# Optimization experiments

Measured on AMD Instinct MI355X. Metric: run time of the kernel, lower is better.

Reference implementation:

```python
import jax, jax.numpy as jnp
import numpy as np

N_HEAD = 16
NEG_INF = jnp.float32(-1e30)


def setup_inputs() -> dict:
    key = jax.random.key(0)
    k1, k2, k3 = jax.random.split(key, 3)
    B, T, C = 2, 2048, 1024
    x = jax.random.normal(k1, (B, T, C), dtype=jnp.float32)
    attn_mask = jnp.ones((B, T), dtype=jnp.int32)
    W_qkv = jax.random.normal(k2, (C, 3 * C), dtype=jnp.float32) * (1.0 / np.sqrt(C))
    b_qkv = jnp.zeros((3 * C,), dtype=jnp.float32)
    W_proj = jax.random.normal(k3, (C, C), dtype=jnp.float32) * (1.0 / np.sqrt(C))
    b_proj = jnp.zeros((C,), dtype=jnp.float32)
    return {"x": x, "attn_mask": attn_mask, "W_qkv": W_qkv, "b_qkv": b_qkv,
            "W_proj": W_proj, "b_proj": b_proj}


def reference(x, attn_mask, W_qkv, b_qkv, W_proj, b_proj):
    B, T, C = x.shape
    H = N_HEAD
    hd = C // H
    qkv = x @ W_qkv + b_qkv                       # [B,T,3C]
    q, k, v = jnp.split(qkv, 3, axis=-1)
    q = q.reshape(B, T, H, hd).transpose(0, 2, 1, 3)  # [B,H,T,hd]
    k = k.reshape(B, T, H, hd).transpose(0, 2, 1, 3)
    v = v.reshape(B, T, H, hd).transpose(0, 2, 1, 3)
    att = jnp.einsum('bhqd,bhkd->bhqk', q, k) / jnp.float32(np.sqrt(hd))  # [B,H,T,T]
    causal = jnp.tril(jnp.ones((T, T), dtype=bool))[None, None]           # [1,1,T,T]
    pad = (attn_mask != 0)[:, None, None, :]                              # [B,1,1,T]
    att = jnp.where(causal & pad, att, NEG_INF)
    att = jax.nn.softmax(att, axis=-1)
    y = jnp.einsum('bhqk,bhkd->bhqd', att, v)     # [B,H,T,hd]
    y = y.transpose(0, 2, 1, 3).reshape(B, T, C)
    return y @ W_proj + b_proj
```

## Files before the change

### kernel.cpp

```cpp
#include <hip/hip_runtime.h>

#define T_SEQ 2048
#define NHEAD 16
#define HD 64
#define CDIM 1024

typedef __bf16 bf16x8 __attribute__((ext_vector_type(8)));
typedef float f32x4 __attribute__((ext_vector_type(4)));
typedef float f32x16 __attribute__((ext_vector_type(16)));

union U16x8 { uint4 u4; unsigned short s[8]; bf16x8 b; };

__device__ __forceinline__ float bf2f(unsigned short u) {
    return __uint_as_float(((unsigned int)u) << 16);
}
__device__ __forceinline__ unsigned short f2bf(float f) {
    unsigned int u = __float_as_uint(f);
    u += 0x7fffu + ((u >> 16) & 1u);
    return (unsigned short)(u >> 16);
}
__device__ __forceinline__ U16x8 load8f(const float* __restrict__ p) {
    U16x8 r;
    float4 f0 = *(const float4*)p;
    float4 f1 = *(const float4*)(p + 4);
    r.s[0] = f2bf(f0.x); r.s[1] = f2bf(f0.y); r.s[2] = f2bf(f0.z); r.s[3] = f2bf(f0.w);
    r.s[4] = f2bf(f1.x); r.s[5] = f2bf(f1.y); r.s[6] = f2bf(f1.z); r.s[7] = f2bf(f1.w);
    return r;
}

__device__ __forceinline__ void async_copy16(const unsigned short* g, unsigned short* l) {
    __builtin_amdgcn_global_load_lds(
        (const __attribute__((address_space(1))) unsigned int*)g,
        (__attribute__((address_space(3))) unsigned int*)l, 16, 0, 0);
}

#define LOG2E 1.442695040f

#define BAR()    asm volatile("s_barrier" ::: "memory")
#define LGKM0()  asm volatile("s_waitcnt lgkmcnt(0)" ::: "memory")
#define VMC6()   asm volatile("s_waitcnt vmcnt(6)" ::: "memory")
#define VMC0()   asm volatile("s_waitcnt vmcnt(0)" ::: "memory")

__device__ __forceinline__ unsigned int cvtpk_bf16(float lo, float hi) {
    unsigned int r;
    asm("v_cvt_pk_bf16_f32 %0, %1, %2" : "=v"(r) : "v"(lo), "v"(hi));
    return r;
}
__device__ __forceinline__ void plane32swap(unsigned int &x, unsigned int &y) {
    asm("v_permlane32_swap_b32 %0, %1" : "+v"(x), "+v"(y));
}

__device__ __forceinline__ void transpose_tile(
    const float* __restrict__ in, unsigned short* __restrict__ out,
    int R, int C, int r0, int c0, float tile[64][65])
{
    const int tid = threadIdx.x;
    const int rr = tid >> 4;
    const int cc = (tid & 15) * 4;
#pragma unroll
    for (int p = 0; p < 4; ++p) {
        float4 v = *(const float4*)&in[(size_t)(r0 + p * 16 + rr) * C + c0 + cc];
        tile[p * 16 + rr][cc] = v.x;
        tile[p * 16 + rr][cc + 1] = v.y;
        tile[p * 16 + rr][cc + 2] = v.z;
        tile[p * 16 + rr][cc + 3] = v.w;
    }
    __syncthreads();
    const int n = tid >> 2;
    const int s = (tid & 3) * 8;
#pragma unroll
    for (int p = 0; p < 2; ++p) {
        const int k = s + p * 32;
        U16x8 o;
#pragma unroll
        for (int j = 0; j < 8; ++j) o.s[j] = f2bf(tile[k + j][n]);
        *(uint4*)&out[(size_t)(c0 + n) * R + r0 + k] = o.u4;
    }
}

__global__ __launch_bounds__(256) void prep(
    const float* __restrict__ X,     unsigned short* __restrict__ Xb,
    const float* __restrict__ Wqkv,  unsigned short* __restrict__ Wqkvt,
    const float* __restrict__ Wproj, unsigned short* __restrict__ Wprojt)
{
    __shared__ float tile[64][65];
    const int bid = blockIdx.x;
    if (bid < 2048) {
        const int i = (bid * 256 + threadIdx.x) * 8;
        U16x8 o = load8f(&X[i]);
        *(uint4*)&Xb[i] = o.u4;
    } else if (bid < 2816) {
        const int u = bid - 2048;
        transpose_tile(Wqkv, Wqkvt, CDIM, 3 * CDIM, (u & 15) * 64, (u >> 4) * 64, tile);
    } else {
        const int u = bid - 2816;
        transpose_tile(Wproj, Wprojt, CDIM, CDIM, (u & 15) * 64, (u >> 4) * 64, tile);
    }
}

__device__ __forceinline__ void gemm128_core(
    const unsigned short* __restrict__ A,
    const unsigned short* __restrict__ Bt,
    int K, int m0, int n0,
    unsigned short* As, unsigned short* Bs, f32x4 acc[4][4])
{
    const int tid = threadIdx.x;
    const int w = tid >> 6, lane = tid & 63;
    const int ln = lane & 15, quad = lane >> 4;
    const int wm = w >> 1, wn = w & 1;
    const int lr = lane >> 3;
    const int lc = (lane & 7) * 8;

    for (int kb = 0; kb < K; kb += 64) {
        __syncthreads();
#pragma unroll
        for (int i = 0; i < 4; ++i) {
            async_copy16(&A[(size_t)(m0 + w * 32 + i * 8 + lr) * K + kb + lc],
                         &As[(w * 32 + i * 8) * 64]);
            async_copy16(&Bt[(size_t)(n0 + w * 32 + i * 8 + lr) * K + kb + lc],
                         &Bs[(w * 32 + i * 8) * 64]);
        }
        __syncthreads();
#pragma unroll
        for (int kk = 0; kk < 2; ++kk) {
            U16x8 af[4], bff[4];
#pragma unroll
            for (int i = 0; i < 4; ++i)
                af[i].u4 = *(const uint4*)&As[(wm * 64 + i * 16 + ln) * 64 + kk * 32 + quad * 8];
#pragma unroll
            for (int j = 0; j < 4; ++j)
                bff[j].u4 = *(const uint4*)&Bs[(wn * 64 + j * 16 + ln) * 64 + kk * 32 + quad * 8];
#pragma unroll
            for (int i = 0; i < 4; ++i)
#pragma unroll
                for (int j = 0; j < 4; ++j)
                    acc[i][j] = __builtin_amdgcn_mfma_f32_16x16x32_bf16(af[i].b, bff[j].b, acc[i][j], 0, 0, 0);
        }
    }
}

__device__ __forceinline__ void stageA(const unsigned short* __restrict__ A,
                                       unsigned short* buf,
                                       int m0, int t, int unit, int w, int lane)
{
#pragma unroll
    for (int s = 0; s < 2; ++s) {
        const int r0 = s * 128 + unit * 64 + w * 8;
        const int row = r0 + (lane >> 3);
        const int col = (16 * (lane & 7)) ^ ((row & 4) ? 32 : 0);
        const unsigned short* src = A + (size_t)(m0 + row) * CDIM + t * 64 + (col >> 1);
        async_copy16(src, buf + r0 * 64);
    }
}

__device__ __forceinline__ void stageB(const unsigned short* __restrict__ B,
                                       unsigned short* buf,
                                       int n0, int t, int unit, int w, int lane)
{
#pragma unroll
    for (int s = 0; s < 2; ++s) {
        const int slice = s * 8 + w;
        const int r0 = (slice >> 2) * 64 + unit * 32 + (slice & 3) * 8;
        const int row = r0 + (lane >> 3);
        const int col = (16 * (lane & 7)) ^ ((row & 4) ? 32 : 0);
        const unsigned short* src = B + (size_t)(n0 + row) * CDIM + t * 64 + (col >> 1);
        async_copy16(src, buf + r0 * 64);
    }
}

__device__ __forceinline__ void readA(U16x8 af[4][2], const unsigned short* buf,
                                      int wm, int qm, int ln, int quad)
{
#pragma unroll
    for (int i = 0; i < 4; ++i) {
        const int row = wm * 128 + qm * 64 + i * 16 + ln;
        const int sw = (row & 4) ? 32 : 0;
#pragma unroll
        for (int kk = 0; kk < 2; ++kk) {
            const int byt = row * 128 + ((kk * 64 + quad * 16) ^ sw);
            af[i][kk].u4 = *(const uint4*)((const char*)buf + byt);
        }
    }
}

__device__ __forceinline__ void readB(U16x8 bf[2][2], const unsigned short* buf,
                                      int wn, int qn, int ln, int quad)
{
#pragma unroll
    for (int jj = 0; jj < 2; ++jj) {
        const int row = wn * 64 + qn * 32 + jj * 16 + ln;
        const int sw = (row & 4) ? 32 : 0;
#pragma unroll
        for (int kk = 0; kk < 2; ++kk) {
            const int byt = row * 128 + ((kk * 64 + quad * 16) ^ sw);
            bf[jj][kk].u4 = *(const uint4*)((const char*)buf + byt);
        }
    }
}

template<int QM, int QN>
__device__ __forceinline__ void mfma16(f32x4 acc[8][4], const U16x8 af[4][2],
                                       const U16x8 bf[2][2])
{
    __builtin_amdgcn_s_setprio(1);
#pragma unroll
    for (int i = 0; i < 4; ++i)
#pragma unroll
        for (int jj = 0; jj < 2; ++jj)
#pragma unroll
            for (int kk = 0; kk < 2; ++kk)
                acc[QM * 4 + i][QN * 2 + jj] = __builtin_amdgcn_mfma_f32_16x16x32_bf16(
                    af[i][kk].b, bf[jj][kk].b, acc[QM * 4 + i][QN * 2 + jj], 0, 0, 0);
    __builtin_amdgcn_s_setprio(0);
}

__global__ __launch_bounds__(512) void qkv8(
    const unsigned short* __restrict__ Xb,
    const unsigned short* __restrict__ Wt,
    const float* __restrict__ bias,
    unsigned short* __restrict__ Qp,
    unsigned short* __restrict__ Kp,
    unsigned short* __restrict__ Vtp)
{
    __shared__ __align__(1024) unsigned short smem[4][16384];
    unsigned short* Ab0 = smem[0];
    unsigned short* Ab1 = smem[1];
    unsigned short* Bb0 = smem[2];
    unsigned short* Bb1 = smem[3];

    const int tid = threadIdx.x;
    const int w = tid >> 6, lane = tid & 63;
    const int ln = lane & 15, quad = lane >> 4;
    const int wm = w >> 2, wn = w & 3;

    const int bid = blockIdx.x;
    const int swz = (bid & 7) * 24 + (bid >> 3);
    const int nt = swz % 12, mt = swz / 12;
    const int m0 = mt * 256, n0 = nt * 256;

    f32x4 acc[8][4];
#pragma unroll
    for (int i = 0; i < 8; ++i)
#pragma unroll
        for (int j = 0; j < 4; ++j) acc[i][j] = (f32x4){0.f, 0.f, 0.f, 0.f};

    stageA(Xb, Ab0, m0, 0, 0, w, lane);
    stageB(Wt, Bb0, n0, 0, 0, w, lane);
    stageB(Wt, Bb0, n0, 0, 1, w, lane);
    stageA(Xb, Ab0, m0, 0, 1, w, lane);
    stageA(Xb, Ab1, m0, 1, 0, w, lane);
    stageB(Wt, Bb1, n0, 1, 0, w, lane);
    stageB(Wt, Bb1, n0, 1, 1, w, lane);
    VMC6();
    BAR();

    U16x8 af[4][2], bq0[2][2], bq1[2][2];

    for (int j = 0; j < 7; ++j) {
        const int e = 2 * j, o = 2 * j + 1;
        readA(af, Ab0, wm, 0, ln, quad);
        readB(bq0, Bb0, wn, 0, ln, quad);
        stageA(Xb, Ab1, m0, o, 1, w, lane);
        BAR(); LGKM0();
        mfma16<0, 0>(acc, af, bq0);
        LGKM0(); BAR();
        readB(bq1, Bb0, wn, 1, ln, quad);
        stageA(Xb, Ab0, m0, e + 2, 0, w, lane);
        BAR(); LGKM0();
        mfma16<0, 1>(acc, af, bq1);
        LGKM0(); BAR();
        readA(af, Ab0, wm, 1, ln, quad);
        stageB(Wt, Bb0, n0, e + 2, 0, w, lane);
        BAR(); LGKM0();
        mfma16<1, 0>(acc, af, bq0);
        LGKM0(); BAR();
        stageB(Wt, Bb0, n0, e + 2, 1, w, lane);
        BAR();
        mfma16<1, 1>(acc, af, bq1);
        VMC6(); BAR();
        readA(af, Ab1, wm, 0, ln, quad);
        readB(bq0, Bb1, wn, 0, ln, quad);
        stageA(Xb, Ab0, m0, e + 2, 1, w, lane);
        BAR(); LGKM0();
        mfma16<0, 0>(acc, af, bq0);
        LGKM0(); BAR();
        readB(bq1, Bb1, wn, 1, ln, quad);
        stageA(Xb, Ab1, m0, o + 2, 0, w, lane);
        BAR(); LGKM0();
        mfma16<0, 1>(acc, af, bq1);
        LGKM0(); BAR();
        readA(af, Ab1, wm, 1, ln, quad);
        stageB(Wt, Bb1, n0, o + 2, 0, w, lane);
        BAR(); LGKM0();
        mfma16<1, 0>(acc, af, bq0);
        LGKM0(); BAR();
        stageB(Wt, Bb1, n0, o + 2, 1, w, lane);
        BAR();
        mfma16<1, 1>(acc, af, bq1);
        VMC6(); BAR();
    }

    stageA(Xb, Ab1, m0, 15, 1, w, lane);
    VMC0(); BAR();

    readA(af, Ab0, wm, 0, ln, quad);
    readB(bq0, Bb0, wn, 0, ln, quad);
    readB(bq1, Bb0, wn, 1, ln, quad);
    mfma16<0, 0>(acc, af, bq0);
    mfma16<0, 1>(acc, af, bq1);
    readA(af, Ab0, wm, 1, ln, quad);
    mfma16<1, 0>(acc, af, bq0);
    mfma16<1, 1>(acc, af, bq1);

    readA(af, Ab1, wm, 0, ln, quad);
    readB(bq0, Bb1, wn, 0, ln, quad);
    readB(bq1, Bb1, wn, 1, ln, quad);
    mfma16<0, 0>(acc, af, bq0);
    mfma16<0, 1>(acc, af, bq1);
    readA(af, Ab1, wm, 1, ln, quad);
    mfma16<1, 0>(acc, af, bq0);
    mfma16<1, 1>(acc, af, bq1);

    const int which = n0 >> 10;
    float bv[4];
#pragma unroll
    for (int jj = 0; jj < 4; ++jj) bv[jj] = bias[n0 + wn * 64 + jj * 16 + ln];

    if (which < 2) {
        unsigned short* dst = (which == 0) ? Qp : Kp;
#pragma unroll
        for (int jj = 0; jj < 4; ++jj) {
            const int n = n0 + wn * 64 + jj * 16 + ln;
            const int h = (n >> 6) & 15, d = n & 63;
#pragma unroll
            for (int i = 0; i < 8; ++i)
#pragma unroll
                for (int r = 0; r < 4; ++r) {
                    const int m = m0 + wm * 128 + i * 16 + quad * 4 + r;
                    const int b = m >> 11, tt = m & 2047;
                    dst[(((size_t)(b * NHEAD + h) * T_SEQ) + tt) * HD + d] =
                        f2bf(acc[i][jj][r] + bv[jj]);
                }
        }
    } else {
#pragma unroll
        for (int jj = 0; jj < 4; ++jj) {
            const int n = n0 + wn * 64 + jj * 16 + ln;
            const int c = n - 2048;
#pragma unroll
            for (int i = 0; i < 8; ++i) {
                const int m00 = m0 + wm * 128 + i * 16 + quad * 4;
                const int b = m00 >> 11, tt = m00 & 2047;
                ushort4 pk;
                pk.x = f2bf(acc[i][jj][0] + bv[jj]);
                pk.y = f2bf(acc[i][jj][1] + bv[jj]);
                pk.z = f2bf(acc[i][jj][2] + bv[jj]);
                pk.w = f2bf(acc[i][jj][3] + bv[jj]);
                *(ushort4*)&Vtp[(size_t)(b * 1024 + c) * T_SEQ + tt] = pk;
            }
        }
    }
}

__global__ __launch_bounds__(256) void proj_gemm(
    const unsigned short* __restrict__ Yin,
    const unsigned short* __restrict__ Wt,
    const float* __restrict__ bias,
    float* __restrict__ out)
{
    __shared__ unsigned short As[128 * 64];
    __shared__ unsigned short Bs[128 * 64];
    const int m0 = blockIdx.y * 128;
    const int n0 = blockIdx.x * 128;

    f32x4 acc[4][4];
#pragma unroll
    for (int i = 0; i < 4; ++i)
#pragma unroll
        for (int j = 0; j < 4; ++j) acc[i][j] = (f32x4){0.f, 0.f, 0.f, 0.f};

    gemm128_core(Yin, Wt, CDIM, m0, n0, As, Bs, acc);

    const int tid = threadIdx.x;
    const int w = tid >> 6, lane = tid & 63;
    const int ln = lane & 15, quad = lane >> 4;
    const int wm = w >> 1, wn = w & 1;

#pragma unroll
    for (int j = 0; j < 4; ++j) {
        const int n = n0 + wn * 64 + j * 16 + ln;
        const float bv = bias[n];
#pragma unroll
        for (int i = 0; i < 4; ++i)
#pragma unroll
            for (int r = 0; r < 4; ++r) {
                const int m = m0 + wm * 64 + i * 16 + quad * 4 + r;
                out[(size_t)m * CDIM + n] = acc[i][j][r] + bv;
            }
    }
}


__device__ __forceinline__ int swz(int row, int slot) {
    return row * 64 + ((slot ^ (row & 7)) << 3);
}

__global__ __launch_bounds__(256) void flash_attn32(
    const unsigned short* __restrict__ Qp,
    const unsigned short* __restrict__ Kp,
    const unsigned short* __restrict__ Vtp,
    const int* __restrict__ mask,
    unsigned short* __restrict__ Y,
    unsigned short* __restrict__ Po,
    float* __restrict__ Pm,
    float* __restrict__ Pl)
{
    __shared__ unsigned short Ks[64 * 64];
    __shared__ unsigned short Vs[64 * 64];
    __shared__ float mask_arr[64];
    __shared__ float als[4][32];
    __shared__ int flagu;

    const int bh = blockIdx.x;
    const int y = blockIdx.y;
    int qb, j0, jstep;
    bool split;
    if (y < 16) { qb = 15 - (y >> 1); j0 = y & 1; jstep = 2; split = true; }
    else        { qb = 23 - y;        j0 = 0;     jstep = 1; split = false; }
    const int sgk = y & 1;

    const int b = bh >> 4, h = bh & 15;
    const int tid = threadIdx.x;
    const int w = tid >> 6, lane = tid & 63;
    const int l31 = lane & 31, hi = lane >> 5;
    const int row8 = tid >> 3, seg = tid & 7;
    const size_t base = (size_t)bh * T_SEQ * HD;
    const int qB = qb * 128;
    const int qw0 = qB + w * 32;
    const int qv = qw0 + l31;
    const int jlast = 2 * qb + 1;

    U16x8 qf[4];
    {
        const unsigned short* qrow = &Qp[base + (size_t)qv * HD];
#pragma unroll
        for (int c = 0; c < 4; ++c)
            qf[c].u4 = *(const uint4*)&qrow[c * 16 + hi * 8];
    }

    f32x16 oA0, oA1;
#pragma unroll
    for (int r = 0; r < 16; ++r) { oA0[r] = 0.f; oA1[r] = 0.f; }
    float m_r = -3.0e38f, mL = 0.f, l_r = 0.f;

    uint4 kr0, kr1, vr0, vr1;
    float mf = 0.f;
    {
        const unsigned short* kp0 = &Kp[base + (size_t)(j0 * 64 + row8) * HD + seg * 8];
        kr0 = *(const uint4*)kp0;
        kr1 = *(const uint4*)(kp0 + 32 * HD);
        const unsigned short* vp0 = &Vtp[base + (size_t)row8 * T_SEQ + j0 * 64 + seg * 8];
        vr0 = *(const uint4*)vp0;
        vr1 = *(const uint4*)(vp0 + 32 * T_SEQ);
        if (tid < 64) mf = mask[b * T_SEQ + j0 * 64 + tid] ? 0.f : -1.0e30f;
    }

    for (int j = j0; j <= jlast; j += jstep) {
        __syncthreads();
        *(uint4*)&Ks[swz(row8, seg)]      = kr0;
        *(uint4*)&Ks[swz(row8 + 32, seg)] = kr1;
        *(uint4*)&Vs[swz(row8, seg)]      = vr0;
        *(uint4*)&Vs[swz(row8 + 32, seg)] = vr1;
        if (w == 0) {
            const int k = lane;
            const int idx = ((k >> 2) & 1) * 32 + (k >> 5) * 16 + ((k & 31) >> 3) * 4 + (k & 3);
            mask_arr[idx] = mf;
            const unsigned long long bb = __ballot(mf == 0.f);
            if (lane == 0) flagu = (bb == 0xFFFFFFFFFFFFFFFFull) ? 0 : 1;
        }
        __syncthreads();

        const int jn = j + jstep;
        if (jn <= jlast) {
            const unsigned short* kp0 = &Kp[base + (size_t)(jn * 64 + row8) * HD + seg * 8];
            kr0 = *(const uint4*)kp0;
            kr1 = *(const uint4*)(kp0 + 32 * HD);
            const unsigned short* vp0 = &Vtp[base + (size_t)row8 * T_SEQ + jn * 64 + seg * 8];
            vr0 = *(const uint4*)vp0;
            vr1 = *(const uint4*)(vp0 + 32 * T_SEQ);
            if (tid < 64) mf = mask[b * T_SEQ + jn * 64 + tid] ? 0.f : -1.0e30f;
        }

        const bool skipw = (j * 64 > qw0 + 31);
        if (!skipw) {
            const bool edge = (j * 64 + 63 > qw0);
            const int anymask = flagu;

            f32x16 sc0, sc1;
#pragma unroll
            for (int r = 0; r < 16; ++r) { sc0[r] = 0.f; sc1[r] = 0.f; }
#pragma unroll
            for (int c = 0; c < 4; ++c) {
                U16x8 ka0, ka1;
                const int r0 = l31, r1 = 32 + l31;
                ka0.u4 = *(const uint4*)&Ks[r0 * 64 + (((2 * c + hi) ^ (r0 & 7)) << 3)];
                ka1.u4 = *(const uint4*)&Ks[r1 * 64 + (((2 * c + hi) ^ (r1 & 7)) << 3)];
                sc0 = __builtin_amdgcn_mfma_f32_32x32x16_bf16(ka0.b, qf[c].b, sc0, 0, 0, 0);
                sc1 = __builtin_amdgcn_mfma_f32_32x32x16_bf16(ka1.b, qf[c].b, sc1, 0, 0, 0);
            }

            if (anymask) {
#pragma unroll
                for (int g = 0; g < 4; ++g) {
                    const f32x4 m0v = *(const f32x4*)&mask_arr[hi * 32 + g * 4];
                    const f32x4 m1v = *(const f32x4*)&mask_arr[hi * 32 + 16 + g * 4];
#pragma unroll
                    for (int t = 0; t < 4; ++t) {
                        sc0[g * 4 + t] = fmaf(sc0[g * 4 + t], 0.125f, m0v[t]);
                        sc1[g * 4 + t] = fmaf(sc1[g * 4 + t], 0.125f, m1v[t]);
                    }
                }
            } else {
#pragma unroll
                for (int r = 0; r < 16; ++r) {
                    sc0[r] *= 0.125f;
                    sc1[r] *= 0.125f;
                }
            }
            if (edge) {
#pragma unroll
                for (int r = 0; r < 16; ++r) {
                    const int krow = (r & 3) + 8 * (r >> 2) + 4 * hi;
                    if (j * 64 + krow > qv)      sc0[r] = -1.0e30f;
                    if (j * 64 + 32 + krow > qv) sc1[r] = -1.0e30f;
                }
            }

            float tm = -3.0e38f;
#pragma unroll
            for (int r = 0; r < 16; ++r)
                tm = fmaxf(tm, fmaxf(sc0[r], sc1[r]));
            tm = fmaxf(tm, __shfl_xor(tm, 32));

            if (__any(tm > m_r + 8.f)) {
                const float mn = fmaxf(m_r, tm);
                const float a = __builtin_amdgcn_exp2f((m_r - mn) * LOG2E);
                m_r = mn; mL = mn * LOG2E;
                l_r *= a;
                if (hi == 0) als[w][l31] = a;
                f32x4 av[4];
#pragma unroll
                for (int g = 0; g < 4; ++g)
                    av[g] = *(const f32x4*)&als[w][g * 8 + hi * 4];
#pragma unroll
                for (int r = 0; r < 16; ++r) {
                    const float aa = av[r >> 2][r & 3];
                    oA0[r] *= aa; oA1[r] *= aa;
                }
            }

            float ps = 0.f;
#pragma unroll
            for (int r = 0; r < 16; ++r) {
                const float p0 = __builtin_amdgcn_exp2f(fmaf(sc0[r], LOG2E, -mL));
                const float p1 = __builtin_amdgcn_exp2f(fmaf(sc1[r], LOG2E, -mL));
                sc0[r] = p0; sc1[r] = p1;
                ps += p0 + p1;
            }
            l_r += ps;

#pragma unroll
            for (int c = 0; c < 4; ++c) {
                const int rb = (c & 1) * 8;
                unsigned int x0, y0, x1, y1;
                if (c < 2) {
                    x0 = cvtpk_bf16(sc0[rb + 0], sc0[rb + 1]);
                    y0 = cvtpk_bf16(sc0[rb + 4], sc0[rb + 5]);
                    x1 = cvtpk_bf16(sc0[rb + 2], sc0[rb + 3]);
                    y1 = cvtpk_bf16(sc0[rb + 6], sc0[rb + 7]);
                } else {
                    x0 = cvtpk_bf16(sc1[rb + 0], sc1[rb + 1]);
                    y0 = cvtpk_bf16(sc1[rb + 4], sc1[rb + 5]);
                    x1 = cvtpk_bf16(sc1[rb + 2], sc1[rb + 3]);
                    y1 = cvtpk_bf16(sc1[rb + 6], sc1[rb + 7]);
                }
                plane32swap(x0, y0);
                plane32swap(x1, y1);
                U16x8 pa;
                pa.u4 = make_uint4(x0, x1, y0, y1);
                {
                    const int vr_0 = l31, vr_1 = 32 + l31;
                    U16x8 vb0, vb1;
                    vb0.u4 = *(const uint4*)&Vs[vr_0 * 64 + (((2 * c + hi) ^ (vr_0 & 7)) << 3)];
                    vb1.u4 = *(const uint4*)&Vs[vr_1 * 64 + (((2 * c + hi) ^ (vr_1 & 7)) << 3)];
                    oA0 = __builtin_amdgcn_mfma_f32_32x32x16_bf16(pa.b, vb0.b, oA0, 0, 0, 0);
                    oA1 = __builtin_amdgcn_mfma_f32_32x32x16_bf16(pa.b, vb1.b, oA1, 0, 0, 0);
                }
            }
        }
    }

    const float lt = l_r + __shfl_xor(l_r, 32);

    if (split) {
        const int pidx = (bh * 8 + (qb - 8)) * 2 + sgk;
        if (hi == 0) {
            Pm[pidx * 128 + w * 32 + l31] = m_r;
            Pl[pidx * 128 + w * 32 + l31] = lt;
        }
#pragma unroll
        for (int r = 0; r < 16; ++r) {
            const int qlc = w * 32 + (r & 3) + 8 * (r >> 2) + 4 * hi;
            Po[(size_t)pidx * 8192 + qlc * 64 + l31]      = f2bf(oA0[r]);
            Po[(size_t)pidx * 8192 + qlc * 64 + 32 + l31] = f2bf(oA1[r]);
        }
    } else {
        if (hi == 0) als[w][l31] = 1.0f / lt;
        f32x4 lv[4];
#pragma unroll
        for (int g = 0; g < 4; ++g)
            lv[g] = *(const f32x4*)&als[w][g * 8 + hi * 4];
#pragma unroll
        for (int r = 0; r < 16; ++r) {
            const int q = qw0 + (r & 3) + 8 * (r >> 2) + 4 * hi;
            const float sl = lv[r >> 2][r & 3];
            const size_t row = (size_t)(b * T_SEQ + q);
            Y[row * CDIM + h * HD + l31]      = f2bf(oA0[r] * sl);
            Y[row * CDIM + h * HD + 32 + l31] = f2bf(oA1[r] * sl);
        }
    }
}

__global__ __launch_bounds__(256) void merge_attn(
    const unsigned short* __restrict__ Po,
    const float* __restrict__ Pm, const float* __restrict__ Pl,
    unsigned short* __restrict__ Y)
{
    const int u = blockIdx.x;
    const int bh = u & 31;
    const int v = u >> 5;
    const int qc = v >> 2, part = v & 3;
    const int tid = threadIdx.x;
    const int ql = part * 32 + (tid >> 3);
    const int d0 = (tid & 7) * 8;
    const int b = bh >> 4, h = bh & 15;
    const int i0 = (bh * 8 + qc) * 2, i1 = i0 + 1;

    const float m0 = Pm[i0 * 128 + ql], m1 = Pm[i1 * 128 + ql];
    const float l0 = Pl[i0 * 128 + ql], l1 = Pl[i1 * 128 + ql];
    const float M = fmaxf(m0, m1);
    const float f0 = __builtin_amdgcn_exp2f((m0 - M) * LOG2E);
    const float f1 = __builtin_amdgcn_exp2f((m1 - M) * LOG2E);
    const float inv = 1.0f / (f0 * l0 + f1 * l1);

    U16x8 a, c, o;
    a.u4 = *(const uint4*)&Po[(size_t)i0 * 8192 + ql * 64 + d0];
    c.u4 = *(const uint4*)&Po[(size_t)i1 * 8192 + ql * 64 + d0];
#pragma unroll
    for (int j = 0; j < 8; ++j)
        o.s[j] = f2bf((f0 * bf2f(a.s[j]) + f1 * bf2f(c.s[j])) * inv);

    const int q = 1024 + qc * 128 + ql;
    *(uint4*)&Y[(size_t)(b * T_SEQ + q) * CDIM + h * HD + d0] = o.u4;
}

extern "C" void kernel_launch(void* const* d_in, const int* in_sizes, int n_in,
                              void* d_out, int out_size, void* d_ws, size_t ws_size,
                              hipStream_t stream)
{
    const float* X     = (const float*)d_in[0];
    const int*   mask  = (const int*)d_in[1];
    const float* Wqkv  = (const float*)d_in[2];
    const float* bqkv  = (const float*)d_in[3];
    const float* Wproj = (const float*)d_in[4];
    const float* bproj = (const float*)d_in[5];
    float* out = (float*)d_out;

    const size_t per = (size_t)2 * NHEAD * T_SEQ * HD;
    unsigned short* Qp     = (unsigned short*)d_ws;
    unsigned short* Kp     = Qp + per;
    unsigned short* Vtp    = Kp + per;
    unsigned short* Xb     = Vtp + per;
    unsigned short* Yp     = Xb;
    unsigned short* Wqkvt  = Xb + per;
    unsigned short* Wprojt = Wqkvt + (size_t)3 * CDIM * CDIM;
    unsigned short* Po     = Wprojt + (size_t)CDIM * CDIM;
    float*          Pm     = (float*)(Po + (size_t)512 * 8192);
    float*          Pl     = Pm + 512 * 128;

    prep<<<3072, 256, 0, stream>>>(X, Xb, Wqkv, Wqkvt, Wproj, Wprojt);
    qkv8<<<192, 512, 0, stream>>>(Xb, Wqkvt, bqkv, Qp, Kp, Vtp);
    flash_attn32<<<dim3(2 * NHEAD, 24), 256, 0, stream>>>(Qp, Kp, Vtp, mask, Yp, Po, Pm, Pl);
    merge_attn<<<1024, 256, 0, stream>>>(Po, Pm, Pl, Yp);
    proj_gemm<<<dim3(8, 32), 256, 0, stream>>>(Yp, Wprojt, bproj, out);
}
```

Before: 213.8 us.

## Process 128-key tiles per sync and fold softmax scale into Q

The flash attention loop now stages 128 keys (two 64-key halves) of K and V into shared memory per iteration, which halves the number of barriers and global-load rounds per query block. The 1/sqrt(hd) scale is folded into the Q projection epilogue, so the per-score scale multiply is removed. Launch bounds now request 2 blocks per CU. The costs are double the shared memory and more registers for prefetching, which may limit occupancy. Q is also rounded to bf16 after scaling, a slight numeric change.

```diff
diff --git a/kernel.cpp b/kernel.cpp
--- a/kernel.cpp
+++ b/kernel.cpp
@@ -328,6 +328,7 @@
 
     if (which < 2) {
         unsigned short* dst = (which == 0) ? Qp : Kp;
+        const float qsc = (which == 0) ? 0.125f : 1.0f;
 #pragma unroll
         for (int jj = 0; jj < 4; ++jj) {
             const int n = n0 + wn * 64 + jj * 16 + ln;
@@ -339,7 +340,7 @@
                     const int m = m0 + wm * 128 + i * 16 + quad * 4 + r;
                     const int b = m >> 11, tt = m & 2047;
                     dst[(((size_t)(b * NHEAD + h) * T_SEQ) + tt) * HD + d] =
-                        f2bf(acc[i][jj][r] + bv[jj]);
+                        f2bf((acc[i][jj][r] + bv[jj]) * qsc);
                 }
         }
     } else {
@@ -405,7 +406,7 @@
     return row * 64 + ((slot ^ (row & 7)) << 3);
 }
 
-__global__ __launch_bounds__(256) void flash_attn32(
+__global__ __launch_bounds__(256, 2) void flash_attn32(
     const unsigned short* __restrict__ Qp,
     const unsigned short* __restrict__ Kp,
     const unsigned short* __restrict__ Vtp,
@@ -415,11 +416,11 @@
     float* __restrict__ Pm,
     float* __restrict__ Pl)
 {
-    __shared__ unsigned short Ks[64 * 64];
-    __shared__ unsigned short Vs[64 * 64];
-    __shared__ float mask_arr[64];
+    __shared__ unsigned short Ks[128 * 64];
+    __shared__ unsigned short Vs[2][64 * 64];
+    __shared__ float mask_arr[128];
     __shared__ float als[4][32];
-    __shared__ int flagu;
+    __shared__ int flagu[2];
 
     const int bh = blockIdx.x;
     const int y = blockIdx.y;
@@ -438,7 +439,7 @@
     const int qB = qb * 128;
     const int qw0 = qB + w * 32;
     const int qv = qw0 + l31;
-    const int jlast = 2 * qb + 1;
+    const int j2last = qb;
 
     U16x8 qf[4];
     {
@@ -453,48 +454,63 @@
     for (int r = 0; r < 16; ++r) { oA0[r] = 0.f; oA1[r] = 0.f; }
     float m_r = -3.0e38f, mL = 0.f, l_r = 0.f;
 
-    uint4 kr0, kr1, vr0, vr1;
+    uint4 kr[4], vr[4];
     float mf = 0.f;
     {
-        const unsigned short* kp0 = &Kp[base + (size_t)(j0 * 64 + row8) * HD + seg * 8];
-        kr0 = *(const uint4*)kp0;
-        kr1 = *(const uint4*)(kp0 + 32 * HD);
-        const unsigned short* vp0 = &Vtp[base + (size_t)row8 * T_SEQ + j0 * 64 + seg * 8];
-        vr0 = *(const uint4*)vp0;
-        vr1 = *(const uint4*)(vp0 + 32 * T_SEQ);
-        if (tid < 64) mf = mask[b * T_SEQ + j0 * 64 + tid] ? 0.f : -1.0e30f;
-    }
-
-    for (int j = j0; j <= jlast; j += jstep) {
+        const unsigned short* kp0 = &Kp[base + (size_t)(j0 * 128 + row8) * HD + seg * 8];
+#pragma unroll
+        for (int i = 0; i < 4; ++i)
+            kr[i] = *(const uint4*)(kp0 + (size_t)(32 * i) * HD);
+#pragma unroll
+        for (int hh = 0; hh < 2; ++hh) {
+            const unsigned short* vp0 = &Vtp[base + (size_t)row8 * T_SEQ + j0 * 128 + hh * 64 + seg * 8];
+            vr[hh * 2]     = *(const uint4*)vp0;
+            vr[hh * 2 + 1] = *(const uint4*)(vp0 + 32 * T_SEQ);
+        }
+        if (tid < 128) mf = mask[b * T_SEQ + j0 * 128 + tid] ? 0.f : -1.0e30f;
+    }
+
+    for (int j2 = j0; j2 <= j2last; j2 += jstep) {
         __syncthreads();
-        *(uint4*)&Ks[swz(row8, seg)]      = kr0;
-        *(uint4*)&Ks[swz(row8 + 32, seg)] = kr1;
-        *(uint4*)&Vs[swz(row8, seg)]      = vr0;
-        *(uint4*)&Vs[swz(row8 + 32, seg)] = vr1;
-        if (w == 0) {
-            const int k = lane;
-            const int idx = ((k >> 2) & 1) * 32 + (k >> 5) * 16 + ((k & 31) >> 3) * 4 + (k & 3);
+#pragma unroll
+        for (int i = 0; i < 4; ++i)
+            *(uint4*)&Ks[swz(row8 + 32 * i, seg)] = kr[i];
+#pragma unroll
+        for (int hh = 0; hh < 2; ++hh) {
+            *(uint4*)&Vs[hh][swz(row8, seg)]      = vr[hh * 2];
+            *(uint4*)&Vs[hh][swz(row8 + 32, seg)] = vr[hh * 2 + 1];
+        }
+        if (w < 2) {
+            const int kk = lane;
+            const int idx = w * 64 + ((kk >> 2) & 1) * 32 + (kk >> 5) * 16
+                          + ((kk & 31) >> 3) * 4 + (kk & 3);
             mask_arr[idx] = mf;
             const unsigned long long bb = __ballot(mf == 0.f);
-            if (lane == 0) flagu = (bb == 0xFFFFFFFFFFFFFFFFull) ? 0 : 1;
+            if (lane == 0) flagu[w] = (bb == 0xFFFFFFFFFFFFFFFFull) ? 0 : 1;
         }
         __syncthreads();
 
-        const int jn = j + jstep;
-        if (jn <= jlast) {
-            const unsigned short* kp0 = &Kp[base + (size_t)(jn * 64 + row8) * HD + seg * 8];
-            kr0 = *(const uint4*)kp0;
-            kr1 = *(const uint4*)(kp0 + 32 * HD);
-            const unsigned short* vp0 = &Vtp[base + (size_t)row8 * T_SEQ + jn * 64 + seg * 8];
-            vr0 = *(const uint4*)vp0;
-            vr1 = *(const uint4*)(vp0 + 32 * T_SEQ);
-            if (tid < 64) mf = mask[b * T_SEQ + jn * 64 + tid] ? 0.f : -1.0e30f;
-        }
-
-        const bool skipw = (j * 64 > qw0 + 31);
-        if (!skipw) {
-            const bool edge = (j * 64 + 63 > qw0);
-            const int anymask = flagu;
+        const int jn = j2 + jstep;
+        if (jn <= j2last) {
+            const unsigned short* kp0 = &Kp[base + (size_t)(jn * 128 + row8) * HD + seg * 8];
+#pragma unroll
+            for (int i = 0; i < 4; ++i)
+                kr[i] = *(const uint4*)(kp0 + (size_t)(32 * i) * HD);
+#pragma unroll
+            for (int hh = 0; hh < 2; ++hh) {
+                const unsigned short* vp0 = &Vtp[base + (size_t)row8 * T_SEQ + jn * 128 + hh * 64 + seg * 8];
+                vr[hh * 2]     = *(const uint4*)vp0;
+                vr[hh * 2 + 1] = *(const uint4*)(vp0 + 32 * T_SEQ);
+            }
+            if (tid < 128) mf = mask[b * T_SEQ + jn * 128 + tid] ? 0.f : -1.0e30f;
+        }
+
+#pragma unroll
+        for (int hh = 0; hh < 2; ++hh) {
+            const int kst = j2 * 128 + hh * 64;
+            if (kst > qw0 + 31) continue;
+            const bool edge = (kst + 63 > qw0);
+            const int anymask = flagu[hh];
 
             f32x16 sc0, sc1;
 #pragma unroll
@@ -502,7 +518,7 @@
 #pragma unroll
             for (int c = 0; c < 4; ++c) {
                 U16x8 ka0, ka1;
-                const int r0 = l31, r1 = 32 + l31;
+                const int r0 = hh * 64 + l31, r1 = hh * 64 + 32 + l31;
                 ka0.u4 = *(const uint4*)&Ks[r0 * 64 + (((2 * c + hi) ^ (r0 & 7)) << 3)];
                 ka1.u4 = *(const uint4*)&Ks[r1 * 64 + (((2 * c + hi) ^ (r1 & 7)) << 3)];
                 sc0 = __builtin_amdgcn_mfma_f32_32x32x16_bf16(ka0.b, qf[c].b, sc0, 0, 0, 0);
@@ -512,27 +528,21 @@
             if (anymask) {
 #pragma unroll
                 for (int g = 0; g < 4; ++g) {
-                    const f32x4 m0v = *(const f32x4*)&mask_arr[hi * 32 + g * 4];
-                    const f32x4 m1v = *(const f32x4*)&mask_arr[hi * 32 + 16 + g * 4];
+                    const f32x4 m0v = *(const f32x4*)&mask_arr[hh * 64 + hi * 32 + g * 4];
+                    const f32x4 m1v = *(const f32x4*)&mask_arr[hh * 64 + hi * 32 + 16 + g * 4];
 #pragma unroll
                     for (int t = 0; t < 4; ++t) {
-                        sc0[g * 4 + t] = fmaf(sc0[g * 4 + t], 0.125f, m0v[t]);
-                        sc1[g * 4 + t] = fmaf(sc1[g * 4 + t], 0.125f, m1v[t]);
+                        sc0[g * 4 + t] += m0v[t];
+                        sc1[g * 4 + t] += m1v[t];
                     }
                 }
-            } else {
-#pragma unroll
-                for (int r = 0; r < 16; ++r) {
-                    sc0[r] *= 0.125f;
-                    sc1[r] *= 0.125f;
-                }
             }
             if (edge) {
 #pragma unroll
                 for (int r = 0; r < 16; ++r) {
                     const int krow = (r & 3) + 8 * (r >> 2) + 4 * hi;
-                    if (j * 64 + krow > qv)      sc0[r] = -1.0e30f;
-                    if (j * 64 + 32 + krow > qv) sc1[r] = -1.0e30f;
+                    if (kst + krow > qv)      sc0[r] = -1.0e30f;
+                    if (kst + 32 + krow > qv) sc1[r] = -1.0e30f;
                 }
             }
 
@@ -591,8 +601,8 @@
                 {
                     const int vr_0 = l31, vr_1 = 32 + l31;
                     U16x8 vb0, vb1;
-                    vb0.u4 = *(const uint4*)&Vs[vr_0 * 64 + (((2 * c + hi) ^ (vr_0 & 7)) << 3)];
-                    vb1.u4 = *(const uint4*)&Vs[vr_1 * 64 + (((2 * c + hi) ^ (vr_1 & 7)) << 3)];
+                    vb0.u4 = *(const uint4*)&Vs[hh][vr_0 * 64 + (((2 * c + hi) ^ (vr_0 & 7)) << 3)];
+                    vb1.u4 = *(const uint4*)&Vs[hh][vr_1 * 64 + (((2 * c + hi) ^ (vr_1 & 7)) << 3)];
                     oA0 = __builtin_amdgcn_mfma_f32_32x32x16_bf16(pa.b, vb0.b, oA0, 0, 0, 0);
                     oA1 = __builtin_amdgcn_mfma_f32_32x32x16_bf16(pa.b, vb1.b, oA1, 0, 0, 0);
                 }
```

Measured after the change: 232.4 us. +8.7%, slower.
